# Kernel tuning notes

Hardware: AMD Instinct MI355X
Metric: run time of the kernel (lower is better)

Reference implementation:

```python
import jax, jax.numpy as jnp
import numpy as np
from jax import lax

N_QUBITS = 10
N_LAYERS = 6
DIM = 1 << N_QUBITS
EPS = 1e-5

_i = np.arange(DIM)
# Z_SIGNS[w, i] = (+1/-1) eigenvalue of PauliZ on wire w (wire 0 = most significant bit)
Z_SIGNS = jnp.asarray(np.stack([1.0 - 2.0 * ((_i >> (N_QUBITS - 1 - w)) & 1) for w in range(N_QUBITS)]).astype(np.float32))

def _layer_perm(r):
    # composed permutation of the ring of CNOT(w, (w+r)%n) gates of one StronglyEntanglingLayers layer
    p = _i.copy()
    for w in range(N_QUBITS):
        c, t = w, (w + r) % N_QUBITS
        pc, pt = N_QUBITS - 1 - c, N_QUBITS - 1 - t
        pg = _i ^ (((_i >> pc) & 1) << pt)
        p = p[pg]
    return p

LAYER_PERMS = [jnp.asarray(_layer_perm(l % (N_QUBITS - 1) + 1), dtype=jnp.int32) for l in range(N_LAYERS)]

def _apply_1q(state, U, wire):
    # state: (B, DIM) complex64; U: (2,2) or batched (B,2,2)
    B = state.shape[0]
    left = 1 << wire
    right = DIM // (2 * left)
    s = state.reshape(B, left, 2, right)
    if U.ndim == 3:
        out = jnp.einsum('bij,bljr->blir', U, s)
    else:
        out = jnp.einsum('ij,bljr->blir', U, s)
    return out.reshape(B, DIM)

def _ry_batched(theta):
    c = jnp.cos(theta / 2)
    s = jnp.sin(theta / 2)
    return jnp.stack([jnp.stack([c, -s], -1), jnp.stack([s, c], -1)], -2).astype(jnp.complex64)

def _rot(phi, theta, omega):
    # PennyLane Rot(phi, theta, omega) = RZ(omega) @ RY(theta) @ RZ(phi)
    c = jnp.cos(theta / 2)
    s = jnp.sin(theta / 2)
    m00 = jnp.exp(-1j * (phi + omega) / 2) * c
    m01 = -jnp.exp(1j * (phi - omega) / 2) * s
    m10 = jnp.exp(-1j * (phi - omega) / 2) * s
    m11 = jnp.exp(1j * (phi + omega) / 2) * c
    return jnp.stack([jnp.stack([m00, m01]), jnp.stack([m10, m11])]).astype(jnp.complex64)

def quantum_forward(xq, qw):
    # batched statevector simulation of: RY(pi*x_i) encoding + StronglyEntanglingLayers
    B = xq.shape[0]
    state = jnp.zeros((B, DIM), jnp.complex64).at[:, 0].set(1.0)
    for w in range(N_QUBITS):
        state = _apply_1q(state, _ry_batched(jnp.pi * xq[:, w]), w)
    for l in range(N_LAYERS):
        for w in range(N_QUBITS):
            state = _apply_1q(state, _rot(qw[l, w, 0], qw[l, w, 1], qw[l, w, 2]), w)
        state = state[:, LAYER_PERMS[l]]
    probs = state.real ** 2 + state.imag ** 2
    return probs @ Z_SIGNS.T  # (B, N_QUBITS) expvals of PauliZ

def _conv(x, w, b):
    y = lax.conv_general_dilated(x, w, (1, 1), 'SAME', dimension_numbers=('NCHW', 'OIHW', 'NCHW'))
    return y + b[None, :, None, None]

def _bn(x, g, b):
    # BatchNorm2d in training mode: per-batch statistics over (N, H, W)
    m = jnp.mean(x, (0, 2, 3), keepdims=True)
    v = jnp.var(x, (0, 2, 3), keepdims=True)
    return (x - m) * lax.rsqrt(v + EPS) * g[None, :, None, None] + b[None, :, None, None]

def _pool(x):
    return lax.reduce_window(x, -jnp.inf, lax.max, (1, 1, 2, 2), (1, 1, 2, 2), 'VALID')

def setup_inputs() -> dict:
    key = jax.random.key(0)
    ks = jax.random.split(key, 16)
    n = lambda k, sh, sc: jax.random.normal(k, sh, jnp.float32) * sc
    return {
        'x': jax.random.normal(ks[0], (256, 3, 64, 64), jnp.float32),
        'conv1_w': n(ks[1], (32, 3, 3, 3), 0.1), 'conv1_b': jnp.zeros(32),
        'bn1_g': jnp.ones(32), 'bn1_b': jnp.zeros(32),
        'conv2_w': n(ks[2], (32, 32, 3, 3), 0.05), 'conv2_b': jnp.zeros(32),
        'bn2_g': jnp.ones(32), 'bn2_b': jnp.zeros(32),
        'conv3_w': n(ks[3], (64, 32, 3, 3), 0.05), 'conv3_b': jnp.zeros(64),
        'bn3_g': jnp.ones(64), 'bn3_b': jnp.zeros(64),
        'conv4_w': n(ks[4], (64, 64, 3, 3), 0.05), 'conv4_b': jnp.zeros(64),
        'bn4_g': jnp.ones(64), 'bn4_b': jnp.zeros(64),
        'fc1_w': n(ks[5], (128, 64 * 16 * 16), 0.01), 'fc1_b': jnp.zeros(128),
        'fc2_w': n(ks[6], (10, 128), 0.05), 'fc2_b': jnp.zeros(10),
        'q_weights': jax.random.uniform(ks[7], (6, 10, 3), jnp.float32),
        'head_w': n(ks[8], (10, 10), 0.1), 'head_b': jnp.zeros(10),
    }

def reference(x, conv1_w, conv1_b, bn1_g, bn1_b, conv2_w, conv2_b, bn2_g, bn2_b,
              conv3_w, conv3_b, bn3_g, bn3_b, conv4_w, conv4_b, bn4_g, bn4_b,
              fc1_w, fc1_b, fc2_w, fc2_b, q_weights, head_w, head_b):
    h = jax.nn.relu(_bn(_conv(x, conv1_w, conv1_b), bn1_g, bn1_b))
    h = jax.nn.relu(_bn(_conv(h, conv2_w, conv2_b), bn2_g, bn2_b))
    h = _pool(h)  # Dropout(0.25) is identity in eval
    h = jax.nn.relu(_bn(_conv(h, conv3_w, conv3_b), bn3_g, bn3_b))
    h = jax.nn.relu(_bn(_conv(h, conv4_w, conv4_b), bn4_g, bn4_b))
    h = _pool(h)
    h = h.reshape(h.shape[0], -1)  # (B, 64*16*16)
    h = jax.nn.relu(h @ fc1_w.T + fc1_b)
    h = h @ fc2_w.T + fc2_b  # (B, n_qubits)
    q = quantum_forward(h, q_weights)
    return q @ head_w.T + head_b  # (B, num_classes)
```

## Files before the change

### kernel.cpp

```cpp
#include <hip/hip_runtime.h>
#include <math.h>

#define PI_F 3.14159265358979323846f

typedef __attribute__((ext_vector_type(8))) _Float16 half8;
typedef __attribute__((ext_vector_type(4))) _Float16 half4;
typedef __attribute__((ext_vector_type(4))) float f32x4;

__global__ __launch_bounds__(256) void prep_kernel(
    const float* __restrict__ x, _Float16* __restrict__ X4,
    const float* __restrict__ w1, const float* __restrict__ w2,
    const float* __restrict__ w3, const float* __restrict__ w4,
    _Float16* __restrict__ t1, _Float16* __restrict__ t2,
    _Float16* __restrict__ t3, _Float16* __restrict__ t4,
    const float* __restrict__ f1w, _Float16* __restrict__ w1t,
    const float* __restrict__ qw, float* __restrict__ rotm,
    unsigned short* __restrict__ perm)
{
    const int b = blockIdx.x;
    const int t = threadIdx.x;
    if (b < 2048) {
        int idx = b * 256 + t;
        int n = idx >> 11;
        int p = (idx & 2047) * 2;
        const float* xb = x + (size_t)n * 12288;
        float2 c0 = *(const float2*)&xb[p];
        float2 c1 = *(const float2*)&xb[4096 + p];
        float2 c2 = *(const float2*)&xb[8192 + p];
        half8 o;
        o[0] = (_Float16)c0.x; o[1] = (_Float16)c1.x; o[2] = (_Float16)c2.x; o[3] = (_Float16)0.f;
        o[4] = (_Float16)c0.y; o[5] = (_Float16)c1.y; o[6] = (_Float16)c2.y; o[7] = (_Float16)0.f;
        *(half8*)&X4[(size_t)idx * 8] = o;
    } else if (b < 2308) {
        int idx = (b - 2048) * 256 + t;
        if (idx < 9216) {
            int j = idx & 7, co = (idx >> 3) & 31, k8 = idx >> 8;
            int k = k8 * 8 + j, tap = k >> 5, ci = k & 31;
            t2[idx] = (_Float16)w2[(size_t)(co * 32 + ci) * 9 + tap];
        } else if (idx < 27648) {
            int e = idx - 9216;
            int j = e & 7, co = (e >> 3) & 31, r = e >> 8;
            int k8 = r % 36, gg = r / 36;
            int k = k8 * 8 + j, tap = k >> 5, ci = k & 31;
            t3[e] = (_Float16)w3[(size_t)((gg * 32 + co) * 32 + ci) * 9 + tap];
        } else if (idx < 64512) {
            int e = idx - 27648;
            int j = e & 7, co = (e >> 3) & 31, r = e >> 8;
            int k8 = r % 36, gc = r / 36;
            int g = gc >> 1, cc = gc & 1;
            int kl = k8 * 8 + j, tap = kl >> 5, ci = cc * 32 + (kl & 31);
            t4[e] = (_Float16)w4[(size_t)((g * 32 + co) * 64 + ci) * 9 + tap];
        } else if (idx < 66560) {
            int e = idx - 64512;
            int j = e & 7, co = (e >> 3) & 31, k8 = e >> 8;
            int k = k8 * 8 + j, tap = k >> 2, ci = k & 3;
            t1[e] = (_Float16)((tap < 9 && ci < 3) ? w1[(size_t)(co * 3 + ci) * 9 + tap] : 0.f);
        }
    } else if (b < 2820) {
        __shared__ float lds[64][65];
        int b2 = b - 2308;
        const int yx0 = (b2 & 3) * 64;
        const int j = b2 >> 2;
        #pragma unroll
        for (int i = 0; i < 16; ++i) {
            int idx = t + 256 * i;
            int c = idx >> 6, yxl = idx & 63;
            lds[c][yxl] = f1w[(size_t)j * 16384 + c * 256 + yx0 + yxl];
        }
        __syncthreads();
        #pragma unroll
        for (int i = 0; i < 2; ++i) {
            int idx = t + 256 * i;
            int yxl = idx >> 3, c8 = idx & 7;
            half8 h;
            #pragma unroll
            for (int jj = 0; jj < 8; ++jj)
                h[jj] = (_Float16)lds[c8 * 8 + jj][yxl];
            *(half8*)&w1t[(size_t)j * 16384 + (size_t)(yx0 + yxl) * 64 + c8 * 8] = h;
        }
    } else {
        if (t < 60) {
            float phi = qw[t * 3], th = qw[t * 3 + 1], om = qw[t * 3 + 2];
            float c = cosf(0.5f * th), s = sinf(0.5f * th);
            float apo = 0.5f * (phi + om), amo = 0.5f * (phi - om);
            float cpo = cosf(apo), spo = sinf(apo);
            float cmo = cosf(amo), smo = sinf(amo);
            rotm[t * 8 + 0] = cpo * c;  rotm[t * 8 + 1] = -spo * c;
            rotm[t * 8 + 2] = -cmo * s; rotm[t * 8 + 3] = -smo * s;
            rotm[t * 8 + 4] = cmo * s;  rotm[t * 8 + 5] = -smo * s;
            rotm[t * 8 + 6] = cpo * c;  rotm[t * 8 + 7] = spo * c;
        }
        for (int e = t; e < 6144; e += 256) {
            int layer = e >> 10, i = e & 1023;
            int r = layer % 9 + 1;
            int jdx = i;
            for (int w = 9; w >= 0; --w) {
                int tt = (w + r) % 10;
                int pc = 9 - w, pt_ = 9 - tt;
                jdx ^= ((jdx >> pc) & 1) << pt_;
            }
            perm[e] = (unsigned short)jdx;
        }
    }
}

__global__ __launch_bounds__(256) void conv1_stats_kernel(
    const _Float16* __restrict__ X4, const _Float16* __restrict__ w1m,
    const float* __restrict__ bias, float* __restrict__ partials)
{
    constexpr int TC = 66, TR = 6;
    constexpr int NPIX = (TR + 1) * TC;
    __shared__ __align__(16) _Float16 s_in[NPIX * 4];
    __shared__ __align__(16) _Float16 s_w[2048];
    __shared__ float s_red[64];

    const int t = threadIdx.x;
    const int row0 = blockIdx.x * 4;
    const int n = blockIdx.z;

    *(half8*)&s_w[t * 8] = *(const half8*)&w1m[t * 8];

    for (int p = t; p < NPIX; p += 256) {
        int col = p % TC, r = p / TC;
        int gy = row0 + r - 1, gx = col - 1;
        uint2 u = make_uint2(0u, 0u);
        if (r < TR && gy >= 0 && gy < 64 && gx >= 0 && gx < 64)
            u = *(const uint2*)&X4[(((size_t)n << 12) + (gy << 6) + gx) * 4];
        *(uint2*)&s_in[p * 4] = u;
    }
    if (t < 64) s_red[t] = 0.f;
    __syncthreads();

    const int w = t >> 6, l = t & 63;
    const int lm = l & 15, lg = l >> 4;
    int pA[4];
    #pragma unroll
    for (int f = 0; f < 4; ++f) {
        int m = w * 64 + f * 16 + lm;
        pA[f] = (m >> 6) * TC + (m & 63);
    }
    f32x4 zero4 = {0.f, 0.f, 0.f, 0.f};
    f32x4 acc[4][2];
    #pragma unroll
    for (int f = 0; f < 4; ++f) { acc[f][0] = zero4; acc[f][1] = zero4; }

    {
        const int t0 = lg * 2;
        const int off0 = (t0 / 3) * TC + (t0 % 3);
        const int off1 = ((t0 + 1) / 3) * TC + ((t0 + 1) % 3);
        half8 b0 = *(const half8*)&s_w[(lg * 32 + lm) * 8];
        half8 b1 = *(const half8*)&s_w[(lg * 32 + 16 + lm) * 8];
        #pragma unroll
        for (int f = 0; f < 4; ++f) {
            half4 alo = *(const half4*)&s_in[(pA[f] + off0) * 4];
            half4 ahi = *(const half4*)&s_in[(pA[f] + off1) * 4];
            half8 a;
            #pragma unroll
            for (int j = 0; j < 4; ++j) { a[j] = alo[j]; a[4 + j] = ahi[j]; }
            acc[f][0] = __builtin_amdgcn_mfma_f32_16x16x32_f16(a, b0, acc[f][0], 0, 0, 0);
            acc[f][1] = __builtin_amdgcn_mfma_f32_16x16x32_f16(a, b1, acc[f][1], 0, 0, 0);
        }
    }
    {
        half8 b0 = *(const half8*)&s_w[((4 + lg) * 32 + lm) * 8];
        half8 b1 = *(const half8*)&s_w[((4 + lg) * 32 + 16 + lm) * 8];
        #pragma unroll
        for (int f = 0; f < 4; ++f) {
            half8 a;
            #pragma unroll
            for (int j = 0; j < 8; ++j) a[j] = (_Float16)0.f;
            if (lg == 0) {
                half4 alo = *(const half4*)&s_in[(pA[f] + 134) * 4];
                half4 ahi = *(const half4*)&s_in[(pA[f] + 198) * 4];
                #pragma unroll
                for (int j = 0; j < 4; ++j) { a[j] = alo[j]; a[4 + j] = ahi[j]; }
            }
            acc[f][0] = __builtin_amdgcn_mfma_f32_16x16x32_f16(a, b0, acc[f][0], 0, 0, 0);
            acc[f][1] = __builtin_amdgcn_mfma_f32_16x16x32_f16(a, b1, acc[f][1], 0, 0, 0);
        }
    }

    float bv0 = bias[lm];
    float bv1 = bias[16 + lm];
    float s0 = 0.f, s20 = 0.f, s1 = 0.f, s21 = 0.f;
    #pragma unroll
    for (int f = 0; f < 4; ++f) {
        #pragma unroll
        for (int r = 0; r < 4; ++r) {
            float v0 = acc[f][0][r] + bv0;
            float v1 = acc[f][1][r] + bv1;
            s0 += v0; s20 += v0 * v0;
            s1 += v1; s21 += v1 * v1;
        }
    }
    s0 += __shfl_xor(s0, 16);  s0 += __shfl_xor(s0, 32);
    s1 += __shfl_xor(s1, 16);  s1 += __shfl_xor(s1, 32);
    s20 += __shfl_xor(s20, 16); s20 += __shfl_xor(s20, 32);
    s21 += __shfl_xor(s21, 16); s21 += __shfl_xor(s21, 32);
    if (l < 16) {
        atomicAdd(&s_red[lm], s0);
        atomicAdd(&s_red[16 + lm], s1);
        atomicAdd(&s_red[32 + lm], s20);
        atomicAdd(&s_red[48 + lm], s21);
    }
    __syncthreads();
    if (t < 64)
        partials[((size_t)n * 16 + blockIdx.x) * 64 + t] = s_red[t];
}

__global__ __launch_bounds__(512, 2) void conv2_fused_kernel(
    const _Float16* __restrict__ X4, const _Float16* __restrict__ w1m,
    const float* __restrict__ c1bias, const _Float16* __restrict__ ssh1,
    const _Float16* __restrict__ wt2, const float* __restrict__ c2bias,
    _Float16* __restrict__ out0, _Float16* __restrict__ out1,
    float* __restrict__ partials)
{
    constexpr int COUT = 32, MF = 4, NB = 2;
    constexpr int ROWS = 8;
    constexpr int TC = 66, NPIX = 10 * 66;
    constexpr int PS = 36;
    constexpr int XC = 68, XPIX = 13 * 68;
    __shared__ __align__(16) _Float16 s_in[NPIX * PS];
    __shared__ __align__(16) _Float16 s_x4[XPIX * 4];
    __shared__ __align__(16) _Float16 s_w1[2048];
    __shared__ float s_red[64];

    const int t = threadIdx.x;
    const int row0 = blockIdx.x * ROWS;
    const int n = blockIdx.z;
    const int w = t >> 6, l = t & 63;
    const int lm = l & 15, lg = l >> 4;

    if (t < 256) *(half8*)&s_w1[t * 8] = *(const half8*)&w1m[t * 8];
    for (int p = t; p < XPIX; p += 512) {
        int c = p % XC, r = p / XC;
        int gy = row0 - 2 + r, gx = c - 2;
        uint2 u = make_uint2(0u, 0u);
        if (gy >= 0 && gy < 64 && gx >= 0 && gx < 64)
            u = *(const uint2*)&X4[(((size_t)n << 12) + (gy << 6) + gx) * 4];
        *(uint2*)&s_x4[p * 4] = u;
    }
    if (t < 64) s_red[t] = 0.f;
    __syncthreads();

    {
        const float b1v0 = c1bias[lm], b1v1 = c1bias[16 + lm];
        const _Float16 sc0 = ssh1[lm], sh0 = ssh1[32 + lm];
        const _Float16 sc1 = ssh1[16 + lm], sh1 = ssh1[48 + lm];
        for (int g = w; g < 42; g += 8) {
            int py = g * 16 + lm;
            int pyc = py < NPIX ? py : 0;
            int ry = pyc / 66, cy = pyc - ry * 66;
            int pb = ry * XC + cy;
            f32x4 a0 = {0.f, 0.f, 0.f, 0.f}, a1 = {0.f, 0.f, 0.f, 0.f};
            {
                const int t0 = lg * 2;
                const int off0 = (t0 / 3) * XC + (t0 % 3);
                const int off1 = ((t0 + 1) / 3) * XC + ((t0 + 1) % 3);
                half8 b0 = *(const half8*)&s_w1[(lg * 32 + lm) * 8];
                half8 b1 = *(const half8*)&s_w1[(lg * 32 + 16 + lm) * 8];
                half4 alo = *(const half4*)&s_x4[(pb + off0) * 4];
                half4 ahi = *(const half4*)&s_x4[(pb + off1) * 4];
                half8 a;
                #pragma unroll
                for (int j = 0; j < 4; ++j) { a[j] = alo[j]; a[4 + j] = ahi[j]; }
                a0 = __builtin_amdgcn_mfma_f32_16x16x32_f16(a, b0, a0, 0, 0, 0);
                a1 = __builtin_amdgcn_mfma_f32_16x16x32_f16(a, b1, a1, 0, 0, 0);
            }
            {
                half8 b0 = *(const half8*)&s_w1[((4 + lg) * 32 + lm) * 8];
                half8 b1 = *(const half8*)&s_w1[((4 + lg) * 32 + 16 + lm) * 8];
                half8 a;
                #pragma unroll
                for (int j = 0; j < 8; ++j) a[j] = (_Float16)0.f;
                if (lg == 0) {
                    half4 alo = *(const half4*)&s_x4[(pb + 138) * 4];
                    half4 ahi = *(const half4*)&s_x4[(pb + 204) * 4];
                    #pragma unroll
                    for (int j = 0; j < 4; ++j) { a[j] = alo[j]; a[4 + j] = ahi[j]; }
                }
                a0 = __builtin_amdgcn_mfma_f32_16x16x32_f16(a, b0, a0, 0, 0, 0);
                a1 = __builtin_amdgcn_mfma_f32_16x16x32_f16(a, b1, a1, 0, 0, 0);
            }
            #pragma unroll
            for (int r2 = 0; r2 < 4; ++r2) {
                int py2 = g * 16 + lg * 4 + r2;
                if (py2 < NPIX) {
                    int r2y = py2 / 66, c2y = py2 - r2y * 66;
                    int gy = row0 - 1 + r2y, gx = c2y - 1;
                    _Float16 y0 = (_Float16)0.f, y1 = (_Float16)0.f;
                    if (gy >= 0 && gy < 64 && gx >= 0 && gx < 64) {
                        _Float16 v0 = (_Float16)(a0[r2] + b1v0);
                        _Float16 v1 = (_Float16)(a1[r2] + b1v1);
                        _Float16 f0 = v0 * sc0 + sh0;
                        _Float16 f1 = v1 * sc1 + sh1;
                        y0 = f0 > (_Float16)0.f ? f0 : (_Float16)0.f;
                        y1 = f1 > (_Float16)0.f ? f1 : (_Float16)0.f;
                    }
                    s_in[py2 * PS + lm] = y0;
                    s_in[py2 * PS + 16 + lm] = y1;
                }
            }
        }
    }
    __syncthreads();

    int pA[MF];
    #pragma unroll
    for (int f = 0; f < MF; ++f)
        pA[f] = w * TC + f * 16 + lm;
    f32x4 zero4 = {0.f, 0.f, 0.f, 0.f};
    f32x4 acc[MF][NB];
    #pragma unroll
    for (int f = 0; f < MF; ++f)
        #pragma unroll
        for (int nb = 0; nb < NB; ++nb) acc[f][nb] = zero4;

    #pragma unroll
    for (int tap = 0; tap < 9; ++tap) {
        const int dy = tap / 3, dx = tap % 3;
        const int poff = dy * TC + dx;
        half8 b[NB];
        #pragma unroll
        for (int nb = 0; nb < NB; ++nb) {
            int col = nb * 16 + lm;
            b[nb] = *(const half8*)&wt2[((tap * 4 + lg) * 32 + col) * 8];
        }
        #pragma unroll
        for (int f = 0; f < MF; ++f) {
            int p = pA[f] + poff;
            half4 alo = *(const half4*)&s_in[p * PS + lg * 8];
            half4 ahi = *(const half4*)&s_in[p * PS + lg * 8 + 4];
            half8 a;
            #pragma unroll
            for (int j = 0; j < 4; ++j) { a[j] = alo[j]; a[4 + j] = ahi[j]; }
            #pragma unroll
            for (int nb = 0; nb < NB; ++nb)
                acc[f][nb] = __builtin_amdgcn_mfma_f32_16x16x32_f16(a, b[nb], acc[f][nb], 0, 0, 0);
        }
    }

    float bv[NB], s[NB], s2[NB];
    #pragma unroll
    for (int nb = 0; nb < NB; ++nb) {
        bv[nb] = c2bias[nb * 16 + lm];
        s[nb] = 0.f; s2[nb] = 0.f;
    }
    #pragma unroll
    for (int f = 0; f < MF; ++f) {
        #pragma unroll
        for (int nb = 0; nb < NB; ++nb) {
            #pragma unroll
            for (int r = 0; r < 4; ++r) {
                float v = acc[f][nb][r] + bv[nb];
                acc[f][nb][r] = v;
                s[nb] += v; s2[nb] += v * v;
            }
        }
    }
    #pragma unroll
    for (int nb = 0; nb < NB; ++nb) {
        s[nb] += __shfl_xor(s[nb], 16);  s[nb] += __shfl_xor(s[nb], 32);
        s2[nb] += __shfl_xor(s2[nb], 16); s2[nb] += __shfl_xor(s2[nb], 32);
    }
    if (l < 16) {
        #pragma unroll
        for (int nb = 0; nb < NB; ++nb) {
            atomicAdd(&s_red[nb * 16 + lm], s[nb]);
            atomicAdd(&s_red[32 + nb * 16 + lm], s2[nb]);
        }
    }

    {
        __syncthreads();
        _Float16* pk = s_in;
        #pragma unroll
        for (int nb = 0; nb < NB; ++nb) {
            #pragma unroll
            for (int f = 0; f < MF; ++f) {
                float v0 = acc[f][nb][0], v1 = acc[f][nb][1];
                float v2 = acc[f][nb][2], v3 = acc[f][nb][3];
                int xp0 = f * 8 + lg * 2;
                int o0 = (w * 32 + xp0) * COUT + nb * 16 + lm;
                int o1 = (w * 32 + xp0 + 1) * COUT + nb * 16 + lm;
                pk[o0] = (_Float16)fminf(v0, v1);
                pk[8192 + o0] = (_Float16)fmaxf(v0, v1);
                pk[o1] = (_Float16)fminf(v2, v3);
                pk[8192 + o1] = (_Float16)fmaxf(v2, v3);
            }
        }
        __syncthreads();
        int hp_row = t >> 7, rem = t & 127;
        int xp = rem >> 2, c8 = rem & 3;
        half8 mnA = *(const half8*)&pk[((2 * hp_row) * 32 + xp) * COUT + c8 * 8];
        half8 mnB = *(const half8*)&pk[((2 * hp_row + 1) * 32 + xp) * COUT + c8 * 8];
        half8 mxA = *(const half8*)&pk[8192 + ((2 * hp_row) * 32 + xp) * COUT + c8 * 8];
        half8 mxB = *(const half8*)&pk[8192 + ((2 * hp_row + 1) * 32 + xp) * COUT + c8 * 8];
        half8 mn, mx;
        #pragma unroll
        for (int j = 0; j < 8; ++j) {
            mn[j] = mnA[j] < mnB[j] ? mnA[j] : mnB[j];
            mx[j] = mxA[j] > mxB[j] ? mxA[j] : mxB[j];
        }
        size_t ob = (((size_t)n * 32 + (row0 >> 1) + hp_row) * 32 + xp) * COUT + c8 * 8;
        *(half8*)&out0[ob] = mn;
        *(half8*)&out1[ob] = mx;
    }

    __syncthreads();
    if (t < 64) {
        size_t bid = (size_t)n * gridDim.x + blockIdx.x;
        partials[bid * 64 + t] = s_red[t];
    }
}

template<int BLOCK, int W, int CIN, int COUT, int MF, int NB,
         bool MMIN, bool POOL>
__global__ __launch_bounds__(BLOCK, (BLOCK == 512 ? 4 : 3)) void conv_mfma_kernel(
    const _Float16* __restrict__ in0, const _Float16* __restrict__ in1,
    const _Float16* __restrict__ coef, const _Float16* __restrict__ wt,
    const float* __restrict__ bias,
    _Float16* __restrict__ out0, _Float16* __restrict__ out1,
    float* __restrict__ partials)
{
    constexpr int H = W;
    constexpr int NWAVE = BLOCK / 64;
    constexpr int SPW = MF * 16;
    constexpr int ROWS = NWAVE * SPW / W;
    constexpr int TR = ROWS + 2;
    constexpr int TC = W + 2;
    constexpr int NPIX = TR * TC;
    constexpr int NCH = CIN / 32;
    constexpr int C8N = CIN / 8;
    constexpr int KC = 288;
    constexpr int COUTB = NB * 16;
    __shared__ __align__(16) _Float16 s_in[NPIX * CIN];
    __shared__ float s_red[2 * COUTB];

    const int t = threadIdx.x;
    const int row0 = blockIdx.x * ROWS;
    const int n = blockIdx.z;

    const int w = t >> 6, l = t & 63;
    const int lm = l & 15, lg = l >> 4;
    int pA[MF];
    #pragma unroll
    for (int f = 0; f < MF; ++f) {
        int m = w * SPW + f * 16 + lm;
        pA[f] = (m / W) * TC + (m % W);
    }
    f32x4 zero4 = {0.f, 0.f, 0.f, 0.f};
    f32x4 acc[MF][NB];
    #pragma unroll
    for (int f = 0; f < MF; ++f)
        #pragma unroll
        for (int nb = 0; nb < NB; ++nb) acc[f][nb] = zero4;
    if (t < 2 * COUTB) s_red[t] = 0.f;

    for (int idx = t; idx < NPIX * C8N; idx += BLOCK) {
        int c8 = idx % C8N;
        int p = idx / C8N;
        int col = p % TC, r = p / TC;
        int gy = row0 + r - 1, gx = col - 1;
        half8 v;
        #pragma unroll
        for (int j = 0; j < 8; ++j) v[j] = (_Float16)0.f;
        if (gy >= 0 && gy < H && gx >= 0 && gx < W) {
            size_t gidx = (((size_t)n * H + gy) * W + gx) * CIN + c8 * 8;
            if (MMIN) {
                half8 mn = *(const half8*)&in0[gidx];
                half8 mx = *(const half8*)&in1[gidx];
                half8 sa = *(const half8*)&coef[c8 * 8];
                half8 sb = *(const half8*)&coef[CIN + c8 * 8];
                half8 sh = *(const half8*)&coef[2 * CIN + c8 * 8];
                #pragma unroll
                for (int j = 0; j < 8; ++j) {
                    _Float16 f = mx[j] * sa[j] + mn[j] * sb[j] + sh[j];
                    v[j] = f > (_Float16)0.f ? f : (_Float16)0.f;
                }
            } else {
                v = *(const half8*)&in0[gidx];
                if (coef) {
                    half8 sc = *(const half8*)&coef[c8 * 8];
                    half8 sh = *(const half8*)&coef[CIN + c8 * 8];
                    #pragma unroll
                    for (int j = 0; j < 8; ++j) {
                        _Float16 f = v[j] * sc[j] + sh[j];
                        v[j] = f > (_Float16)0.f ? f : (_Float16)0.f;
                    }
                }
            }
        }
        *(half8*)&s_in[(c8 * NPIX + p) * 8] = v;
    }
    __syncthreads();

    #pragma unroll
    for (int tap = 0; tap < 9; ++tap) {
        const int dy = tap / 3, dx = tap % 3;
        const int poff = dy * TC + dx;
        #pragma unroll
        for (int cc = 0; cc < NCH; ++cc) {
            half8 b[NB];
            #pragma unroll
            for (int nb = 0; nb < NB; ++nb) {
                int cog = nb * 16 + lm;
                int gg = cog >> 5, col = cog & 31;
                const _Float16* wp = wt + (size_t)(gg * NCH + cc) * KC * 32;
                b[nb] = *(const half8*)&wp[((tap * 4 + lg) * 32 + col) * 8];
            }
            #pragma unroll
            for (int f = 0; f < MF; ++f) {
                half8 a = *(const half8*)&s_in[((cc * 4 + lg) * NPIX + pA[f] + poff) * 8];
                #pragma unroll
                for (int nb = 0; nb < NB; ++nb)
                    acc[f][nb] = __builtin_amdgcn_mfma_f32_16x16x32_f16(a, b[nb], acc[f][nb], 0, 0, 0);
            }
        }
    }

    float bv[NB], s[NB], s2[NB];
    #pragma unroll
    for (int nb = 0; nb < NB; ++nb) {
        bv[nb] = bias[nb * 16 + lm];
        s[nb] = 0.f; s2[nb] = 0.f;
    }
    #pragma unroll
    for (int f = 0; f < MF; ++f) {
        #pragma unroll
        for (int r = 0; r < 4; ++r) {
            int m = w * SPW + f * 16 + lg * 4 + r;
            int yy = row0 + m / W, xo = m % W;
            size_t base = (((size_t)n * H + yy) * W + xo) * COUT;
            #pragma unroll
            for (int nb = 0; nb < NB; ++nb) {
                float v = acc[f][nb][r] + bv[nb];
                if (!POOL) out0[base + nb * 16 + lm] = (_Float16)v;
                s[nb] += v; s2[nb] += v * v;
            }
        }
    }
    #pragma unroll
    for (int nb = 0; nb < NB; ++nb) {
        s[nb] += __shfl_xor(s[nb], 16);  s[nb] += __shfl_xor(s[nb], 32);
        s2[nb] += __shfl_xor(s2[nb], 16); s2[nb] += __shfl_xor(s2[nb], 32);
    }
    if (l < 16) {
        #pragma unroll
        for (int nb = 0; nb < NB; ++nb) {
            atomicAdd(&s_red[nb * 16 + lm], s[nb]);
            atomicAdd(&s_red[COUTB + nb * 16 + lm], s2[nb]);
        }
    }

    if (POOL) {
        constexpr int FH = MF / 2;
        constexpr int PPIX = (ROWS / 2) * (W / 2);
        static_assert(2 * PPIX * COUT <= NPIX * CIN, "pool pack fits in s_in");
        __syncthreads();
        _Float16* pk = s_in;
        #pragma unroll
        for (int nb = 0; nb < NB; ++nb) {
            #pragma unroll
            for (int f = 0; f < FH; ++f) {
                #pragma unroll
                for (int rp = 0; rp < 2; ++rp) {
                    float a0 = acc[f][nb][2 * rp] + bv[nb];
                    float a1 = acc[f][nb][2 * rp + 1] + bv[nb];
                    float a2 = acc[f + FH][nb][2 * rp] + bv[nb];
                    float a3 = acc[f + FH][nb][2 * rp + 1] + bv[nb];
                    float mn = fminf(fminf(a0, a1), fminf(a2, a3));
                    float mx = fmaxf(fmaxf(a0, a1), fmaxf(a2, a3));
                    int xp = f * 8 + lg * 2 + rp;
                    int o = (w * (W / 2) + xp) * COUT + nb * 16 + lm;
                    pk[o] = (_Float16)mn;
                    pk[PPIX * COUT + o] = (_Float16)mx;
                }
            }
        }
        __syncthreads();
        size_t gb = (((size_t)n * (H / 2) + (row0 >> 1)) * (W / 2)) * COUT;
        for (int idx = t; idx < PPIX * COUT / 8; idx += BLOCK) {
            *(half8*)&out0[gb + (size_t)idx * 8] = *(const half8*)&pk[idx * 8];
            *(half8*)&out1[gb + (size_t)idx * 8] = *(const half8*)&pk[(PPIX * COUT + idx * 8)];
        }
    }

    __syncthreads();
    if (t < 2 * COUTB) {
        size_t bid = (size_t)n * gridDim.x + blockIdx.x;
        partials[bid * 2 * COUTB + t] = s_red[t];
    }
}

__global__ __launch_bounds__(256) void bn_finalize_kernel(
    const float* __restrict__ partials, int nx, float inv_count,
    const float* __restrict__ gamma, const float* __restrict__ beta,
    float* __restrict__ ss, _Float16* __restrict__ ssh,
    _Float16* __restrict__ sab, int COUT)
{
    const int c = blockIdx.x;
    const int t = threadIdx.x;
    float sum = 0.f, sq = 0.f;
    int total = 256 * nx;
    for (int e = t; e < total; e += 256) {
        size_t off = (size_t)e * 2 * COUT;
        sum += partials[off + c];
        sq  += partials[off + COUT + c];
    }
    #pragma unroll
    for (int off = 32; off > 0; off >>= 1) {
        sum += __shfl_xor(sum, off);
        sq  += __shfl_xor(sq, off);
    }
    __shared__ float rs[4], rq[4];
    if ((t & 63) == 0) { rs[t >> 6] = sum; rq[t >> 6] = sq; }
    __syncthreads();
    if (t == 0) {
        sum = rs[0] + rs[1] + rs[2] + rs[3];
        sq  = rq[0] + rq[1] + rq[2] + rq[3];
        float mean = sum * inv_count;
        float var = sq * inv_count - mean * mean;
        float scale = gamma[c] * rsqrtf(var + 1e-5f);
        float shift = beta[c] - mean * scale;
        ss[c] = scale;
        ss[COUT + c] = shift;
        if (ssh) {
            ssh[c] = (_Float16)scale;
            ssh[COUT + c] = (_Float16)shift;
        }
        if (sab) {
            sab[c] = (_Float16)(scale > 0.f ? scale : 0.f);
            sab[COUT + c] = (_Float16)(scale > 0.f ? 0.f : scale);
            sab[2 * COUT + c] = (_Float16)shift;
        }
    }
}

__global__ __launch_bounds__(256) void fc1_mfma_kernel(
    const _Float16* __restrict__ Amin, const _Float16* __restrict__ Amax,
    const _Float16* __restrict__ sab, const _Float16* __restrict__ Bw,
    float* __restrict__ hp)
{
    __shared__ __align__(16) _Float16 As[64][72];
    __shared__ __align__(16) _Float16 Bs[128][72];
    const int t = threadIdx.x;
    const int mt = blockIdx.x;
    const int kc = blockIdx.y;
    const int w = t >> 6, l = t & 63;
    const int lm = l & 15, lg = l >> 4;

    f32x4 zero4 = {0.f, 0.f, 0.f, 0.f};
    f32x4 acc[8];
    #pragma unroll
    for (int nb = 0; nb < 8; ++nb) acc[nb] = zero4;

    const size_t a_base = (size_t)(mt * 64) * 16384 + (size_t)kc * 512;
    const size_t b_base = (size_t)kc * 512;

    for (int p = 0; p < 8; ++p) {
        __syncthreads();
        #pragma unroll
        for (int i = 0; i < 2; ++i) {
            int idx = t + 256 * i;
            int r = idx >> 3, c8 = idx & 7;
            size_t off = a_base + (size_t)r * 16384 + p * 64 + c8 * 8;
            half8 mn = *(const half8*)&Amin[off];
            half8 mx = *(const half8*)&Amax[off];
            half8 sa = *(const half8*)&sab[c8 * 8];
            half8 sb = *(const half8*)&sab[64 + c8 * 8];
            half8 sh = *(const half8*)&sab[128 + c8 * 8];
            half8 v;
            #pragma unroll
            for (int j = 0; j < 8; ++j) {
                _Float16 f = mx[j] * sa[j] + mn[j] * sb[j] + sh[j];
                v[j] = f > (_Float16)0.f ? f : (_Float16)0.f;
            }
            *(half8*)&As[r][c8 * 8] = v;
        }
        #pragma unroll
        for (int i = 0; i < 4; ++i) {
            int idx = t + 256 * i;
            int r = idx >> 3, c8 = idx & 7;
            *(half8*)&Bs[r][c8 * 8] =
                *(const half8*)&Bw[b_base + (size_t)r * 16384 + p * 64 + c8 * 8];
        }
        __syncthreads();
        #pragma unroll
        for (int ks = 0; ks < 64; ks += 32) {
            half8 a = *(const half8*)&As[w * 16 + lm][ks + lg * 8];
            #pragma unroll
            for (int nb = 0; nb < 8; ++nb) {
                half8 b = *(const half8*)&Bs[nb * 16 + lm][ks + lg * 8];
                acc[nb] = __builtin_amdgcn_mfma_f32_16x16x32_f16(a, b, acc[nb], 0, 0, 0);
            }
        }
    }
    #pragma unroll
    for (int nb = 0; nb < 8; ++nb) {
        #pragma unroll
        for (int r = 0; r < 4; ++r) {
            int row = mt * 64 + w * 16 + lg * 4 + r;
            hp[((size_t)kc * 256 + row) * 128 + nb * 16 + lm] = acc[nb][r];
        }
    }
}

__global__ __launch_bounds__(128) void fcq_kernel(
    const float* __restrict__ hp, const float* __restrict__ f1b,
    const float* __restrict__ f2w, const float* __restrict__ f2b,
    const float* __restrict__ rotm, const unsigned short* __restrict__ perm,
    const float* __restrict__ head_w, const float* __restrict__ head_b,
    float* __restrict__ outp)
{
    __shared__ float lds[2048];
    __shared__ float hl[128];
    __shared__ float xql[10];
    const int n = blockIdx.x;
    const int t = threadIdx.x;

    {
        float s = f1b[t];
        #pragma unroll
        for (int kc = 0; kc < 32; ++kc) s += hp[((size_t)kc * 256 + n) * 128 + t];
        hl[t] = fmaxf(0.f, s);
    }
    __syncthreads();
    if (t < 10) {
        float o = f2b[t];
        #pragma unroll 4
        for (int k = 0; k < 128; ++k) o += f2w[t * 128 + k] * hl[k];
        xql[t] = o;
    }
    __syncthreads();
    if (t >= 64) return;

    const int l = t;
    float ar[16], ai[16];
    #pragma unroll
    for (int r = 0; r < 16; ++r) { ar[r] = 0.f; ai[r] = 0.f; }
    if (l == 0) ar[0] = 1.f;

    #pragma unroll
    for (int w = 0; w < 10; ++w) {
        float th = 0.5f * PI_F * xql[w];
        float c = cosf(th), s = sinf(th);
        const int k = 9 - w;
        if (k >= 6) {
            const int b = k - 6;
            #pragma unroll
            for (int r = 0; r < 16; ++r) {
                if (!(r & (1 << b))) {
                    int r1 = r | (1 << b);
                    float a0 = ar[r], a1 = ar[r1];
                    ar[r]  = c * a0 - s * a1;
                    ar[r1] = s * a0 + c * a1;
                }
            }
        } else {
            float ss = ((l >> k) & 1) ? s : -s;
            #pragma unroll
            for (int r = 0; r < 16; ++r) {
                float p = __shfl_xor(ar[r], 1 << k);
                ar[r] = c * ar[r] + ss * p;
            }
        }
    }

    #pragma unroll 1
    for (int layer = 0; layer < 6; ++layer) {
        #pragma unroll
        for (int w = 0; w < 10; ++w) {
            const float* m = rotm + (layer * 10 + w) * 8;
            float m00r = m[0], m00i = m[1], m01r = m[2], m01i = m[3];
            float m10r = m[4], m10i = m[5], m11r = m[6], m11i = m[7];
            const int k = 9 - w;
            if (k >= 6) {
                const int b = k - 6;
                #pragma unroll
                for (int r = 0; r < 16; ++r) {
                    if (!(r & (1 << b))) {
                        int r1 = r | (1 << b);
                        float a0r = ar[r], a0i = ai[r];
                        float a1r = ar[r1], a1i = ai[r1];
                        ar[r]  = m00r * a0r - m00i * a0i + m01r * a1r - m01i * a1i;
                        ai[r]  = m00r * a0i + m00i * a0r + m01r * a1i + m01i * a1r;
                        ar[r1] = m10r * a0r - m10i * a0i + m11r * a1r - m11i * a1i;
                        ai[r1] = m10r * a0i + m10i * a0r + m11r * a1i + m11i * a1r;
                    }
                }
            } else {
                int bit = (l >> k) & 1;
                float mAr = bit ? m11r : m00r, mAi = bit ? m11i : m00i;
                float mBr = bit ? m10r : m01r, mBi = bit ? m10i : m01i;
                #pragma unroll
                for (int r = 0; r < 16; ++r) {
                    float pr = __shfl_xor(ar[r], 1 << k);
                    float pi = __shfl_xor(ai[r], 1 << k);
                    float mr = ar[r], mi = ai[r];
                    ar[r] = mAr * mr - mAi * mi + mBr * pr - mBi * pi;
                    ai[r] = mAr * mi + mAi * mr + mBr * pi + mBi * pr;
                }
            }
        }
        #pragma unroll
        for (int r = 0; r < 16; ++r) {
            lds[(r << 6) | l] = ar[r];
            lds[1024 + ((r << 6) | l)] = ai[r];
        }
        __syncthreads();
        const unsigned short* pt = perm + layer * 1024;
        #pragma unroll
        for (int r = 0; r < 16; ++r) {
            int ji = pt[(r << 6) | l];
            ar[r] = lds[ji];
            ai[r] = lds[1024 + ji];
        }
        __syncthreads();
    }

    float S = 0.f, T0 = 0.f, T1 = 0.f, T2 = 0.f, T3 = 0.f;
    #pragma unroll
    for (int r = 0; r < 16; ++r) {
        float pr = ar[r] * ar[r] + ai[r] * ai[r];
        S += pr;
        T0 += (r & 1) ? -pr : pr;
        T1 += (r & 2) ? -pr : pr;
        T2 += (r & 4) ? -pr : pr;
        T3 += (r & 8) ? -pr : pr;
    }
    float pk[10];
    pk[0] = T3; pk[1] = T2; pk[2] = T1; pk[3] = T0;
    #pragma unroll
    for (int w = 4; w < 10; ++w)
        pk[w] = ((l >> (9 - w)) & 1) ? -S : S;
    #pragma unroll
    for (int w = 0; w < 10; ++w) {
        #pragma unroll
        for (int off = 1; off < 64; off <<= 1)
            pk[w] += __shfl_xor(pk[w], off);
    }
    if (l < 10) {
        float o = head_b[l];
        #pragma unroll
        for (int kk = 0; kk < 10; ++kk) o += pk[kk] * head_w[l * 10 + kk];
        outp[n * 10 + l] = o;
    }
}

extern "C" void kernel_launch(void* const* d_in, const int* in_sizes, int n_in,
                              void* d_out, int out_size, void* d_ws, size_t ws_size,
                              hipStream_t stream)
{
    const float* x   = (const float*)d_in[0];
    const float* c1w = (const float*)d_in[1];  const float* c1b = (const float*)d_in[2];
    const float* g1  = (const float*)d_in[3];  const float* b1  = (const float*)d_in[4];
    const float* c2w = (const float*)d_in[5];  const float* c2b = (const float*)d_in[6];
    const float* g2  = (const float*)d_in[7];  const float* b2  = (const float*)d_in[8];
    const float* c3w = (const float*)d_in[9];  const float* c3b = (const float*)d_in[10];
    const float* g3  = (const float*)d_in[11]; const float* b3  = (const float*)d_in[12];
    const float* c4w = (const float*)d_in[13]; const float* c4b = (const float*)d_in[14];
    const float* g4  = (const float*)d_in[15]; const float* b4  = (const float*)d_in[16];
    const float* f1w = (const float*)d_in[17]; const float* f1b = (const float*)d_in[18];
    const float* f2w = (const float*)d_in[19]; const float* f2b = (const float*)d_in[20];
    const float* qw  = (const float*)d_in[21];
    const float* hw  = (const float*)d_in[22]; const float* hb  = (const float*)d_in[23];

    float* ws = (float*)d_ws;
    _Float16* H0 = (_Float16*)ws;
    _Float16* H1 = H0 + 33554432;
    float* part = ws + 33554432;
    float* ss1  = part + 524288;
    float* ss2  = ss1 + 64;
    float* ss3  = ss2 + 64;
    float* ss4  = ss3 + 128;
    float* hp   = ss4 + 128;
    float* rotm = hp + 1048576;
    unsigned short* perm16 = (unsigned short*)(rotm + 480);
    _Float16* ssh1 = (_Float16*)(perm16 + 6144);
    _Float16* ssh3 = ssh1 + 64;
    _Float16* sab2 = ssh3 + 128;
    _Float16* sab4 = sab2 + 96;
    _Float16* wt2  = sab4 + 192;
    _Float16* wt3  = wt2 + 9216;
    _Float16* wt4  = wt3 + 18432;
    _Float16* w1m  = wt4 + 36864;
    _Float16* w1t  = w1m + 2048;
    _Float16* X4   = w1t + 2097152;

    _Float16* minT2 = H1;
    _Float16* maxT2 = H1 + 8388608;
    _Float16* minT4 = H1;
    _Float16* maxT4 = H1 + 4194304;

    prep_kernel<<<2821, 256, 0, stream>>>(x, X4, c1w, c2w, c3w, c4w,
                                          w1m, wt2, wt3, wt4, f1w, w1t,
                                          qw, rotm, perm16);

    conv1_stats_kernel<<<dim3(16, 1, 256), 256, 0, stream>>>(X4, w1m, c1b, part);
    bn_finalize_kernel<<<32, 256, 0, stream>>>(part, 16, 1.f / 1048576.f,
                                               g1, b1, ss1, ssh1, nullptr, 32);

    conv2_fused_kernel<<<dim3(8, 1, 256), 512, 0, stream>>>(
        X4, w1m, c1b, ssh1, wt2, c2b, minT2, maxT2, part);
    bn_finalize_kernel<<<32, 256, 0, stream>>>(part, 8, 1.f / 1048576.f,
                                               g2, b2, ss2, nullptr, sab2, 32);

    conv_mfma_kernel<512, 32, 32, 64, 4, 4, true, false>
        <<<dim3(2, 1, 256), 512, 0, stream>>>(
        minT2, maxT2, sab2, wt3, c3b, H0, nullptr, part);
    bn_finalize_kernel<<<64, 256, 0, stream>>>(part, 2, 1.f / 262144.f,
                                               g3, b3, ss3, ssh3, nullptr, 64);

    conv_mfma_kernel<512, 32, 64, 64, 4, 4, false, true>
        <<<dim3(2, 1, 256), 512, 0, stream>>>(
        H0, nullptr, ssh3, wt4, c4b, minT4, maxT4, part);
    bn_finalize_kernel<<<64, 256, 0, stream>>>(part, 2, 1.f / 262144.f,
                                               g4, b4, ss4, nullptr, sab4, 64);

    fc1_mfma_kernel<<<dim3(4, 32), 256, 0, stream>>>(minT4, maxT4, sab4, w1t, hp);

    fcq_kernel<<<256, 128, 0, stream>>>(hp, f1b, f2w, f2b,
                                        rotm, perm16, hw, hb, (float*)d_out);
}
```

Measured before the change: 196.4 us.

## Pre-pad input image in global memory and read conv1 taps directly from global

The prep kernel now writes the fp16 4-channel input into a zero-padded 70x68 layout per image, so the halo bounds checks disappear from the conv loaders. The conv2 fused kernel drops its LDS staging of the input patch and reads conv1 im2col operands straight from global (cache-backed) memory, which frees LDS. Launch bounds are raised to allow six blocks per CU for higher occupancy. In exchange, global-load latency now sits in the MFMA inner loop, and the padded buffer adds some extra write traffic in prep.

```diff
diff --git a/kernel.cpp b/kernel.cpp
--- a/kernel.cpp
+++ b/kernel.cpp
@@ -8,7 +8,7 @@
 typedef __attribute__((ext_vector_type(4))) float f32x4;
 
 __global__ __launch_bounds__(256) void prep_kernel(
-    const float* __restrict__ x, _Float16* __restrict__ X4,
+    const float* __restrict__ x, _Float16* __restrict__ X4P,
     const float* __restrict__ w1, const float* __restrict__ w2,
     const float* __restrict__ w3, const float* __restrict__ w4,
     _Float16* __restrict__ t1, _Float16* __restrict__ t2,
@@ -19,20 +19,29 @@
 {
     const int b = blockIdx.x;
     const int t = threadIdx.x;
-    if (b < 2048) {
-        int idx = b * 256 + t;
-        int n = idx >> 11;
-        int p = (idx & 2047) * 2;
-        const float* xb = x + (size_t)n * 12288;
-        float2 c0 = *(const float2*)&xb[p];
-        float2 c1 = *(const float2*)&xb[4096 + p];
-        float2 c2 = *(const float2*)&xb[8192 + p];
+    if (b < 2380) {
+        int pp = (b * 256 + t) * 2;
         half8 o;
-        o[0] = (_Float16)c0.x; o[1] = (_Float16)c1.x; o[2] = (_Float16)c2.x; o[3] = (_Float16)0.f;
-        o[4] = (_Float16)c0.y; o[5] = (_Float16)c1.y; o[6] = (_Float16)c2.y; o[7] = (_Float16)0.f;
-        *(half8*)&X4[(size_t)idx * 8] = o;
-    } else if (b < 2308) {
-        int idx = (b - 2048) * 256 + t;
+        #pragma unroll
+        for (int j = 0; j < 2; ++j) {
+            int p = pp + j;
+            int n = p / 4760;
+            int rem = p - n * 4760;
+            int yp = rem / 68, xp = rem - (rem / 68) * 68;
+            int gy = yp - 2, gx = xp - 2;
+            float v0 = 0.f, v1 = 0.f, v2 = 0.f;
+            if (gy >= 0 && gy < 64 && gx >= 0 && gx < 64) {
+                const float* xb = x + (size_t)n * 12288 + gy * 64 + gx;
+                v0 = xb[0]; v1 = xb[4096]; v2 = xb[8192];
+            }
+            o[j * 4 + 0] = (_Float16)v0;
+            o[j * 4 + 1] = (_Float16)v1;
+            o[j * 4 + 2] = (_Float16)v2;
+            o[j * 4 + 3] = (_Float16)0.f;
+        }
+        *(half8*)&X4P[(size_t)pp * 4] = o;
+    } else if (b < 2640) {
+        int idx = (b - 2380) * 256 + t;
         if (idx < 9216) {
             int j = idx & 7, co = (idx >> 3) & 31, k8 = idx >> 8;
             int k = k8 * 8 + j, tap = k >> 5, ci = k & 31;
@@ -56,9 +65,9 @@
             int k = k8 * 8 + j, tap = k >> 2, ci = k & 3;
             t1[e] = (_Float16)((tap < 9 && ci < 3) ? w1[(size_t)(co * 3 + ci) * 9 + tap] : 0.f);
         }
-    } else if (b < 2820) {
+    } else if (b < 3152) {
         __shared__ float lds[64][65];
-        int b2 = b - 2308;
+        int b2 = b - 2640;
         const int yx0 = (b2 & 3) * 64;
         const int j = b2 >> 2;
         #pragma unroll
@@ -105,7 +114,7 @@
 }
 
 __global__ __launch_bounds__(256) void conv1_stats_kernel(
-    const _Float16* __restrict__ X4, const _Float16* __restrict__ w1m,
+    const _Float16* __restrict__ X4P, const _Float16* __restrict__ w1m,
     const float* __restrict__ bias, float* __restrict__ partials)
 {
     constexpr int TC = 66, TR = 6;
@@ -122,10 +131,11 @@
 
     for (int p = t; p < NPIX; p += 256) {
         int col = p % TC, r = p / TC;
-        int gy = row0 + r - 1, gx = col - 1;
         uint2 u = make_uint2(0u, 0u);
-        if (r < TR && gy >= 0 && gy < 64 && gx >= 0 && gx < 64)
-            u = *(const uint2*)&X4[(((size_t)n << 12) + (gy << 6) + gx) * 4];
+        if (r < TR) {
+            size_t pb = ((size_t)(n * 70 + row0 + r + 1) * 68 + col + 1) * 4;
+            u = *(const uint2*)&X4P[pb];
+        }
         *(uint2*)&s_in[p * 4] = u;
     }
     if (t < 64) s_red[t] = 0.f;
@@ -208,8 +218,8 @@
         partials[((size_t)n * 16 + blockIdx.x) * 64 + t] = s_red[t];
 }
 
-__global__ __launch_bounds__(512, 2) void conv2_fused_kernel(
-    const _Float16* __restrict__ X4, const _Float16* __restrict__ w1m,
+__global__ __launch_bounds__(512, 6) void conv2_fused_kernel(
+    const _Float16* __restrict__ X4P, const _Float16* __restrict__ w1m,
     const float* __restrict__ c1bias, const _Float16* __restrict__ ssh1,
     const _Float16* __restrict__ wt2, const float* __restrict__ c2bias,
     _Float16* __restrict__ out0, _Float16* __restrict__ out1,
@@ -219,9 +229,8 @@
     constexpr int ROWS = 8;
     constexpr int TC = 66, NPIX = 10 * 66;
     constexpr int PS = 36;
-    constexpr int XC = 68, XPIX = 13 * 68;
+    constexpr int XC = 68;
     __shared__ __align__(16) _Float16 s_in[NPIX * PS];
-    __shared__ __align__(16) _Float16 s_x4[XPIX * 4];
     __shared__ __align__(16) _Float16 s_w1[2048];
     __shared__ float s_red[64];
 
@@ -231,15 +240,9 @@
     const int w = t >> 6, l = t & 63;
     const int lm = l & 15, lg = l >> 4;
 
+    const _Float16* Xb = X4P + ((size_t)(n * 70 + row0) * 68) * 4;
+
     if (t < 256) *(half8*)&s_w1[t * 8] = *(const half8*)&w1m[t * 8];
-    for (int p = t; p < XPIX; p += 512) {
-        int c = p % XC, r = p / XC;
-        int gy = row0 - 2 + r, gx = c - 2;
-        uint2 u = make_uint2(0u, 0u);
-        if (gy >= 0 && gy < 64 && gx >= 0 && gx < 64)
-            u = *(const uint2*)&X4[(((size_t)n << 12) + (gy << 6) + gx) * 4];
-        *(uint2*)&s_x4[p * 4] = u;
-    }
     if (t < 64) s_red[t] = 0.f;
     __syncthreads();
 
@@ -259,8 +262,8 @@
                 const int off1 = ((t0 + 1) / 3) * XC + ((t0 + 1) % 3);
                 half8 b0 = *(const half8*)&s_w1[(lg * 32 + lm) * 8];
                 half8 b1 = *(const half8*)&s_w1[(lg * 32 + 16 + lm) * 8];
-                half4 alo = *(const half4*)&s_x4[(pb + off0) * 4];
-                half4 ahi = *(const half4*)&s_x4[(pb + off1) * 4];
+                half4 alo = *(const half4*)&Xb[(size_t)(pb + off0) * 4];
+                half4 ahi = *(const half4*)&Xb[(size_t)(pb + off1) * 4];
                 half8 a;
                 #pragma unroll
                 for (int j = 0; j < 4; ++j) { a[j] = alo[j]; a[4 + j] = ahi[j]; }
@@ -274,8 +277,8 @@
                 #pragma unroll
                 for (int j = 0; j < 8; ++j) a[j] = (_Float16)0.f;
                 if (lg == 0) {
-                    half4 alo = *(const half4*)&s_x4[(pb + 138) * 4];
-                    half4 ahi = *(const half4*)&s_x4[(pb + 204) * 4];
+                    half4 alo = *(const half4*)&Xb[(size_t)(pb + 138) * 4];
+                    half4 ahi = *(const half4*)&Xb[(size_t)(pb + 204) * 4];
                     #pragma unroll
                     for (int j = 0; j < 4; ++j) { a[j] = alo[j]; a[4 + j] = ahi[j]; }
                 }
@@ -886,23 +889,23 @@
     _Float16* wt4  = wt3 + 18432;
     _Float16* w1m  = wt4 + 36864;
     _Float16* w1t  = w1m + 2048;
-    _Float16* X4   = w1t + 2097152;
+    _Float16* X4P  = w1t + 2097152;
 
     _Float16* minT2 = H1;
     _Float16* maxT2 = H1 + 8388608;
     _Float16* minT4 = H1;
     _Float16* maxT4 = H1 + 4194304;
 
-    prep_kernel<<<2821, 256, 0, stream>>>(x, X4, c1w, c2w, c3w, c4w,
+    prep_kernel<<<3153, 256, 0, stream>>>(x, X4P, c1w, c2w, c3w, c4w,
                                           w1m, wt2, wt3, wt4, f1w, w1t,
                                           qw, rotm, perm16);
 
-    conv1_stats_kernel<<<dim3(16, 1, 256), 256, 0, stream>>>(X4, w1m, c1b, part);
+    conv1_stats_kernel<<<dim3(16, 1, 256), 256, 0, stream>>>(X4P, w1m, c1b, part);
     bn_finalize_kernel<<<32, 256, 0, stream>>>(part, 16, 1.f / 1048576.f,
                                                g1, b1, ss1, ssh1, nullptr, 32);
 
     conv2_fused_kernel<<<dim3(8, 1, 256), 512, 0, stream>>>(
-        X4, w1m, c1b, ssh1, wt2, c2b, minT2, maxT2, part);
+        X4P, w1m, c1b, ssh1, wt2, c2b, minT2, maxT2, part);
     bn_finalize_kernel<<<32, 256, 0, stream>>>(part, 8, 1.f / 1048576.f,
                                                g2, b2, ss2, nullptr, sab2, 32);
 
```

Result: no change. 194.0 us (-1.2%).
